# Optimization experiments

Measured on AMD Instinct MI355X. Metric: run time of the kernel, lower is better.

The kernel has to match this reference:

```python
import jax, jax.numpy as jnp
import numpy as np

EPS = 1e-5

def conv1d_same(x, w, b):
    # x: [B,C,T], w: [O,I,K], b: [O]
    y = jax.lax.conv_general_dilated(x, w, window_strides=(1,), padding='SAME',
                                     dimension_numbers=('NCH', 'OIH', 'NCH'))
    return y + b[None, :, None]

def bn_eval(x, gamma, beta):
    # running_mean=0, running_var=1 (fresh BatchNorm1d in eval mode)
    inv = 1.0 / jnp.sqrt(1.0 + EPS)
    return x * (gamma * inv)[None, :, None] + beta[None, :, None]

def gelu(x):
    return jax.nn.gelu(x, approximate=False)

def conv_block(x, c1w, c1b, c2w, c2b, g1, be1, g2, be2, skw=None, skb=None):
    res = x if skw is None else jnp.einsum('bct,oc->bot', x, skw[:, :, 0]) + skb[None, :, None]
    h = gelu(bn_eval(conv1d_same(x, c1w, c1b), g1, be1))
    h = bn_eval(conv1d_same(h, c2w, c2b), g2, be2)
    return gelu(h + res)

def setup_inputs() -> dict:
    key = jax.random.key(0)
    ks = jax.random.split(key, 32)
    B, C, T = 1024, 271, 281
    H, H2, E, NCLS, NSUBJ = 128, 256, 16, 1854, 4
    g = lambda i, shape, s=0.02: jax.random.normal(ks[i], shape, dtype=jnp.float32) * s
    inp = {}
    inp['X'] = jax.random.normal(ks[0], (B, C, T), dtype=jnp.float32)
    inp['subject_idxs'] = jax.random.randint(ks[1], (B,), 0, NSUBJ, dtype=jnp.int32)
    inp['attention'] = jax.random.normal(ks[2], (C, C), dtype=jnp.float32)
    inp['sa_w'] = g(3, (H, C), 0.05)
    inp['sa_b'] = jnp.zeros((H,), jnp.float32)
    inp['subj_w'] = g(4, (NSUBJ, H, H), 0.05)
    inp['subj_b'] = jnp.zeros((NSUBJ, H), jnp.float32)
    # block1: 128->128 (identity skip)
    inp['b1_c1w'] = g(5, (H, H, 3)); inp['b1_c1b'] = jnp.zeros((H,), jnp.float32)
    inp['b1_c2w'] = g(6, (H, H, 3)); inp['b1_c2b'] = jnp.zeros((H,), jnp.float32)
    inp['b1_g1'] = jnp.ones((H,), jnp.float32); inp['b1_be1'] = jnp.zeros((H,), jnp.float32)
    inp['b1_g2'] = jnp.ones((H,), jnp.float32); inp['b1_be2'] = jnp.zeros((H,), jnp.float32)
    # block2: 128->256 (1x1 conv skip)
    inp['b2_c1w'] = g(7, (H2, H, 3)); inp['b2_c1b'] = jnp.zeros((H2,), jnp.float32)
    inp['b2_c2w'] = g(8, (H2, H2, 3)); inp['b2_c2b'] = jnp.zeros((H2,), jnp.float32)
    inp['b2_g1'] = jnp.ones((H2,), jnp.float32); inp['b2_be1'] = jnp.zeros((H2,), jnp.float32)
    inp['b2_g2'] = jnp.ones((H2,), jnp.float32); inp['b2_be2'] = jnp.zeros((H2,), jnp.float32)
    inp['b2_skw'] = g(9, (H2, H, 1)); inp['b2_skb'] = jnp.zeros((H2,), jnp.float32)
    # block3: 256->256 (identity skip)
    inp['b3_c1w'] = g(10, (H2, H2, 3)); inp['b3_c1b'] = jnp.zeros((H2,), jnp.float32)
    inp['b3_c2w'] = g(11, (H2, H2, 3)); inp['b3_c2b'] = jnp.zeros((H2,), jnp.float32)
    inp['b3_g1'] = jnp.ones((H2,), jnp.float32); inp['b3_be1'] = jnp.zeros((H2,), jnp.float32)
    inp['b3_g2'] = jnp.ones((H2,), jnp.float32); inp['b3_be2'] = jnp.zeros((H2,), jnp.float32)
    # subject embedding + head
    inp['emb'] = g(12, (NSUBJ, E), 1.0)
    inp['head_w1'] = g(13, (H, H2 + E), 0.05); inp['head_b1'] = jnp.zeros((H,), jnp.float32)
    inp['head_w2'] = g(14, (NCLS, H), 0.05); inp['head_b2'] = jnp.zeros((NCLS,), jnp.float32)
    return inp

def reference(X, subject_idxs, attention, sa_w, sa_b, subj_w, subj_b,
              b1_c1w, b1_c1b, b1_c2w, b1_c2b, b1_g1, b1_be1, b1_g2, b1_be2,
              b2_c1w, b2_c1b, b2_c2w, b2_c2b, b2_g1, b2_be1, b2_g2, b2_be2, b2_skw, b2_skb,
              b3_c1w, b3_c1b, b3_c2w, b3_c2b, b3_g1, b3_be1, b3_g2, b3_be2,
              emb, head_w1, head_b1, head_w2, head_b2):
    # SpatialAttention
    attn = jax.nn.softmax(attention, axis=1)            # [C,C]
    x = jnp.einsum('bct,ic->bit', X, attn)              # [B,C,T]
    x = jnp.einsum('bit,oi->bot', x, sa_w) + sa_b[None, :, None]  # [B,H,T]
    # Per-subject 1x1 conv: batched gather of weights instead of python loop
    Ws = subj_w[subject_idxs]                           # [B,H,H]
    bs = subj_b[subject_idxs]                           # [B,H]
    x = jnp.einsum('bct,boc->bot', x, Ws) + bs[:, :, None]
    # ConvBlock stack
    x = conv_block(x, b1_c1w, b1_c1b, b1_c2w, b1_c2b, b1_g1, b1_be1, b1_g2, b1_be2)
    x = conv_block(x, b2_c1w, b2_c1b, b2_c2w, b2_c2b, b2_g1, b2_be1, b2_g2, b2_be2, b2_skw, b2_skb)
    x = conv_block(x, b3_c1w, b3_c1b, b3_c2w, b3_c2b, b3_g1, b3_be1, b3_g2, b3_be2)
    # Head: global avg pool over time, concat subject embedding, MLP
    x = jnp.mean(x, axis=2)                             # [B,2H]
    x = jnp.concatenate([x, emb[subject_idxs]], axis=1) # [B,2H+E]
    h = jax.nn.relu(x @ head_w1.T + head_b1)
    return h @ head_w2.T + head_b2                      # [B,num_classes]
```

## Files before the change

kernel.cpp:

```cpp
#include <hip/hip_runtime.h>
#include <hip/hip_bf16.h>
#include <math.h>

constexpr int Bz = 1024;
constexpr int C0 = 271;
constexpr int CP0 = 288;
constexpr int Tt = 281;
constexpr int TR = 292;
constexpr int H1 = 128;
constexpr int H2 = 256;
constexpr int NCLS = 1854;
constexpr int ED = 16;
constexpr float BN_INV = 0.9999950000374996f;

typedef __attribute__((ext_vector_type(8))) short s16x8;
typedef __attribute__((ext_vector_type(16))) float f32x16;

__device__ __forceinline__ float gelu_f(float v) {
    return 0.5f * v * (1.0f + erff(v * 0.7071067811865475f));
}
__device__ __forceinline__ float bf2f(short s) {
    return __builtin_bit_cast(float, ((unsigned int)(unsigned short)s) << 16);
}
__device__ __forceinline__ short f2bf(float f) {
    return __builtin_bit_cast(short, __float2bfloat16(f));
}

typedef unsigned int u32;
typedef const __attribute__((address_space(1))) u32 gu32;
typedef __attribute__((address_space(3))) u32 lu32;

__device__ __forceinline__ void gl16(const void* g, void* l) {
    __builtin_amdgcn_global_load_lds((gu32*)(uintptr_t)g, (lu32*)(uintptr_t)l, 16, 0, 0);
}
template<int N> __device__ __forceinline__ void waitv() {
    asm volatile("s_waitcnt vmcnt(%0)" :: "i"(N) : "memory");
}
__device__ __forceinline__ void hard_barrier() {
    __builtin_amdgcn_sched_barrier(0);
    __builtin_amdgcn_s_barrier();
    __builtin_amdgcn_sched_barrier(0);
}


__global__ void zrows_k(short* base, int C) {
    const int b = blockIdx.x;
    const int n = 11 * (C / 8);
    for (int i = threadIdx.x; i < n; i += 256) {
        int ri = i / (C / 8), c8 = i - ri * (C / 8);
        int row = (ri == 0) ? 0 : 281 + ri;
        *(int4*)(base + ((size_t)b * TR + row) * C + c8 * 8) = make_int4(0, 0, 0, 0);
    }
}

__global__ void softmax_rows_k(const float* __restrict__ a, float* __restrict__ o, int n) {
    __shared__ float red[256];
    const int row = blockIdx.x, tid = threadIdx.x;
    const float* r = a + (size_t)row * n;
    float m = -1e30f;
    for (int i = tid; i < n; i += 256) m = fmaxf(m, r[i]);
    red[tid] = m; __syncthreads();
    for (int s = 128; s > 0; s >>= 1) { if (tid < s) red[tid] = fmaxf(red[tid], red[tid + s]); __syncthreads(); }
    m = red[0]; __syncthreads();
    float acc = 0.f;
    for (int i = tid; i < n; i += 256) acc += expf(r[i] - m);
    red[tid] = acc; __syncthreads();
    for (int s = 128; s > 0; s >>= 1) { if (tid < s) red[tid] += red[tid + s]; __syncthreads(); }
    const float inv = 1.0f / red[0];
    for (int i = tid; i < n; i += 256) o[(size_t)row * n + i] = expf(r[i] - m) * inv;
}

__global__ void gemm_M_k(const float* __restrict__ sa_w, const float* __restrict__ attnS,
                         float* __restrict__ M) {
    int idx = blockIdx.x * 256 + threadIdx.x;
    if (idx >= H1 * C0) return;
    int o = idx / C0, c = idx - o * C0;
    float s = 0.f;
    for (int i = 0; i < C0; ++i) s = fmaf(sa_w[(size_t)o * C0 + i], attnS[(size_t)i * C0 + c], s);
    M[idx] = s;
}

__global__ void wfrag_k(const float* __restrict__ w, short* __restrict__ out,
                        int CIN, int O, int K, int NC) {
    int idx = blockIdx.x * 256 + threadIdx.x;
    int OB32 = O / 32;
    int total = NC * K * OB32 * 2 * 512;
    if (idx >= total) return;
    int j = idx & 7, lane = (idx >> 3) & 63, kk = (idx >> 9) & 1, r = idx >> 10;
    int ob = r % OB32, r2 = r / OB32;
    int k = r2 % K, cc = r2 / K;
    int o = ob * 32 + (lane & 31);
    int c = cc * 32 + kk * 16 + (lane >> 5) * 8 + j;
    float v = (c < CIN) ? w[((size_t)o * CIN + c) * K + k] : 0.f;
    out[idx] = f2bf(v);
}

__global__ void msubA_k(const float* __restrict__ subj_w, const float* __restrict__ M,
                        short* __restrict__ out) {
    int idx = blockIdx.x * 256 + threadIdx.x;
    const int per_s = 9 * 1 * 4 * 2 * 512;
    if (idx >= 4 * per_s) return;
    int s = idx / per_s, rem = idx % per_s;
    int j = rem & 7, lane = (rem >> 3) & 63, kk = (rem >> 9) & 1, r = rem >> 10;
    int ob = r % 4, cc = r / 4;
    int o = ob * 32 + (lane & 31);
    int c = cc * 32 + kk * 16 + (lane >> 5) * 8 + j;
    float a = 0.f;
    if (c < C0) {
        const float* wr = subj_w + ((size_t)s * 128 + o) * 128;
        for (int h = 0; h < 128; ++h) a = fmaf(wr[h], M[(size_t)h * C0 + c], a);
    }
    out[idx] = f2bf(a);
}

__global__ void biasS_k(const float* __restrict__ subj_w, const float* __restrict__ sa_b,
                        const float* __restrict__ subj_b, float* __restrict__ biasS) {
    int idx = blockIdx.x * 256 + threadIdx.x;
    if (idx >= 4 * H1) return;
    int s = idx >> 7, o = idx & 127;
    const float* wr = subj_w + ((size_t)s * H1 + o) * H1;
    float a = subj_b[idx];
    for (int h = 0; h < H1; ++h) a = fmaf(wr[h], sa_b[h], a);
    biasS[idx] = a;
}

__global__ void xpose_k(const float* __restrict__ X, short* __restrict__ xT) {
    __shared__ float tile[32][33];
    int b = blockIdx.z;
    int t0 = blockIdx.x * 32, c0 = blockIdx.y * 32;
    int tx = threadIdx.x, ty = threadIdx.y;
    #pragma unroll
    for (int i = 0; i < 4; ++i) {
        int c = c0 + ty + i * 8, t = t0 + tx;
        float v = 0.f;
        if (c < C0 && t < Tt) v = X[((size_t)b * C0 + c) * Tt + t];
        tile[ty + i * 8][tx] = v;
    }
    __syncthreads();
    #pragma unroll
    for (int i = 0; i < 4; ++i) {
        int t = t0 + ty + i * 8, c = c0 + tx;
        if (t < Tt) xT[((size_t)b * TR + t + 1) * CP0 + c] = f2bf(tile[tx][ty + i * 8]);
    }
}


template<int NCCp, int ROWUp, int NW, int NCH>
__device__ __forceinline__ void conv_stage(
    const short* slabg, int XC, int cubase, char* lds, int wv, int lane)
{
    constexpr int ROWB = ROWUp * 16;
    for (int i = wv; i < NCH; i += NW) {
        int pos = i * 1024 + lane * 16;
        int rl = pos / ROWB;
        int up = (pos - rl * ROWB) >> 4;
        if (rl > 291) rl = 291;
        int ul = up ^ (rl & 7);
        int srcu = (ul < NCCp * 4) ? ul : 0;
        gl16(slabg + (size_t)rl * XC + (cubase + srcu) * 8, lds + i * 1024);
    }
}

template<int K, int CCB, int NPH, int ROWU, int OB32>
__device__ __forceinline__ void conv_phases(
    f32x16 (&acc)[2][3], const short* __restrict__ wb, const char* Xb,
    int tg, int lane, int l31, int hi, int wvo)
{
    constexpr int ROWB = ROWU * 16;
    constexpr int ROFF = 1 - (K - 1) / 2;
    s16x8 ab[2][4];
    #pragma unroll
    for (int i = 0; i < 4; ++i) {
        int ci = ((CCB * K + 0) * OB32 + wvo * 2 + (i >> 1)) * 2 + (i & 1);
        ab[0][i] = *(const s16x8*)(wb + (size_t)ci * 512 + lane * 8);
    }
    #pragma unroll
    for (int p = 0; p < NPH; ++p) {
        const int k  = p % K;
        const int cl = p / K;
        if (p + 1 < NPH) {
            const int cn = CCB + (p + 1) / K, kn = (p + 1) % K;
            #pragma unroll
            for (int i = 0; i < 4; ++i) {
                int ci = ((cn * K + kn) * OB32 + wvo * 2 + (i >> 1)) * 2 + (i & 1);
                ab[(p + 1) & 1][i] = *(const s16x8*)(wb + (size_t)ci * 512 + lane * 8);
            }
        }
        s16x8 bf[2][3];
        #pragma unroll
        for (int kk = 0; kk < 2; ++kk)
            #pragma unroll
            for (int ts = 0; ts < 3; ++ts) {
                int rl = tg + ts * 32 + l31 + k + ROFF;
                bf[kk][ts] = *(const s16x8*)(Xb + (size_t)rl * ROWB +
                               (((cl * 4 + kk * 2 + hi) ^ (rl & 7)) << 4));
            }
        hard_barrier();
        __builtin_amdgcn_s_setprio(1);
        #pragma unroll
        for (int ts = 0; ts < 3; ++ts)
            #pragma unroll
            for (int kk = 0; kk < 2; ++kk) {
                acc[0][ts] = __builtin_amdgcn_mfma_f32_32x32x16_bf16(ab[p & 1][kk],     bf[kk][ts], acc[0][ts], 0, 0, 0);
                acc[1][ts] = __builtin_amdgcn_mfma_f32_32x32x16_bf16(ab[p & 1][2 + kk], bf[kk][ts], acc[1][ts], 0, 0, 0);
            }
        __builtin_amdgcn_s_setprio(0);
        hard_barrier();
    }
}

template<int K, int NCC_A, int ROWU_A, int NCC_B, int ROWU_B,
         int O_BLK, int NOW, int NB, bool GELU, bool HASRES, bool POOL>
__global__ __launch_bounds__(NOW * NB * 192)
void convPH(const short* __restrict__ xin, int XC,
            const short* __restrict__ wfrag,
            const float* __restrict__ bias,
            const float* __restrict__ gamma, const float* __restrict__ beta,
            const short* __restrict__ res, short* __restrict__ outp,
            float* __restrict__ pooled,
            const int* __restrict__ sidx, int wsub, int bsub)
{
    constexpr int NW    = NOW * NB * 3;
    constexpr int NT    = NW * 64;
    constexpr int OB32  = O_BLK / 32;
    constexpr int SLABB = ((292 * ROWU_A * 16) + 1023) & ~1023;
    constexpr int NCH_A = SLABB / 1024;
    constexpr int NCH_B = (292 * ROWU_B * 16 + 1023) / 1024;
    constexpr int O2    = O_BLK * 2;

    __shared__ __align__(16) char smem[NB * SLABB];

    const int b0   = blockIdx.x * NB;
    const int tid  = threadIdx.x;
    const int lane = tid & 63, wv = tid >> 6;
    const int l31  = lane & 31, hi = lane >> 5;
    const int bqw  = wv / (NOW * 3);
    const int w2   = wv % (NOW * 3);
    const int wvt  = w2 / NOW;
    const int wvo  = w2 % NOW;
    const int tg   = wvt * 96;

    int subj = sidx ? sidx[b0] : 0;
    const short* wb = wfrag + (size_t)subj * wsub;
    const float* bb = bias + (size_t)subj * bsub;

    f32x16 acc[2][3];
    #pragma unroll
    for (int i = 0; i < 2; ++i)
        #pragma unroll
        for (int j = 0; j < 3; ++j)
            #pragma unroll
            for (int e = 0; e < 16; ++e) acc[i][j][e] = 0.f;

    #pragma unroll
    for (int b = 0; b < NB; ++b)
        conv_stage<NCC_A, ROWU_A, NW, NCH_A>(
            xin + (size_t)(b0 + b) * TR * XC, XC, 0, smem + b * SLABB, wv, lane);
    waitv<0>();
    hard_barrier();

    const char* Xb = smem + bqw * SLABB;
    conv_phases<K, 0, NCC_A * K, ROWU_A, OB32>(acc, wb, Xb, tg, lane, l31, hi, wvo);

    if constexpr (NCC_B > 0) {
        #pragma unroll
        for (int b = 0; b < NB; ++b)
            conv_stage<NCC_B, ROWU_B, NW, NCH_B>(
                xin + (size_t)(b0 + b) * TR * XC, XC, NCC_A * 4, smem + b * SLABB, wv, lane);
        waitv<0>();
        hard_barrier();
        conv_phases<K, NCC_A, NCC_B * K, ROWU_B, OB32>(acc, wb, Xb, tg, lane, l31, hi, wvo);
    }

    constexpr int RCH = O_BLK / 8;
    float ps[8];
    if constexpr (POOL) {
        #pragma unroll
        for (int j = 0; j < 8; ++j) ps[j] = 0.f;
    }
    for (int g = 0; g < 3; ++g) {
        __syncthreads();
        if (wvt == g) {
            #pragma unroll
            for (int os = 0; os < 2; ++os) {
                #pragma unroll
                for (int rq = 0; rq < 4; ++rq) {
                    #pragma unroll
                    for (int rp = 0; rp < 2; ++rp) {
                        const int oc = wvo * 64 + os * 32 + 8 * rq + rp * 2 + 4 * hi;
                        const float bv0 = bb[oc], bv1 = bb[oc + 1];
                        const float g0 = gamma ? gamma[oc] * BN_INV : 1.f;
                        const float g1 = gamma ? gamma[oc + 1] * BN_INV : 1.f;
                        const float e0 = beta ? beta[oc] : 0.f;
                        const float e1 = beta ? beta[oc + 1] : 0.f;
                        const int r0 = rq * 4 + rp * 2;
                        #pragma unroll
                        for (int ts = 0; ts < 3; ++ts) {
                            float v0 = (acc[os][ts][r0] + bv0) * g0 + e0;
                            float v1 = (acc[os][ts][r0 + 1] + bv1) * g1 + e1;
                            int tl = ts * 32 + l31;
                            int byte = (bqw * 96 + tl) * O2 + ((oc * 2) ^ ((tl & 15) << 4));
                            __hip_bfloat162 pk;
                            pk.x = __float2bfloat16(v0);
                            pk.y = __float2bfloat16(v1);
                            *(__hip_bfloat162*)(smem + byte) = pk;
                        }
                    }
                }
            }
        }
        __syncthreads();
        for (int qq = tid; qq < NB * 96 * RCH; qq += NT) {
            int bql = qq / (96 * RCH), rem = qq - bql * (96 * RCH);
            int r = rem / RCH, cp = rem - r * RCH;
            int t = g * 96 + r;
            if (t >= Tt) continue;
            s16x8 hv = *(const s16x8*)(smem + (bql * 96 + r) * O2 + ((cp * 16) ^ ((r & 15) << 4)));
            size_t orow = ((size_t)(b0 + bql) * TR + t + 1) * O_BLK + cp * 8;
            s16x8 rv;
            if (HASRES) rv = *(const s16x8*)(res + orow);
            if constexpr (POOL) {
                #pragma unroll
                for (int j = 0; j < 8; ++j) {
                    float v = bf2f(hv[j]);
                    if (HASRES) v += bf2f(rv[j]);
                    if (GELU) v = gelu_f(v);
                    ps[j] += v;
                }
            } else {
                s16x8 ov;
                #pragma unroll
                for (int j = 0; j < 8; ++j) {
                    float v = bf2f(hv[j]);
                    if (HASRES) v += bf2f(rv[j]);
                    if (GELU) v = gelu_f(v);
                    ov[j] = f2bf(v);
                }
                *(s16x8*)(outp + orow) = ov;
            }
        }
    }

    if constexpr (POOL) {
        constexpr int NRED = NT / RCH;
        float* part = (float*)(smem + 96 * (size_t)O2);
        __syncthreads();
        #pragma unroll
        for (int j = 0; j < 8; ++j) part[tid * 8 + j] = ps[j];
        __syncthreads();
        if (tid < O_BLK) {
            int cp = tid >> 3, j = tid & 7;
            float s = 0.f;
            for (int r = 0; r < NRED; ++r) s += part[(cp + RCH * r) * 8 + j];
            pooled[(size_t)b0 * H2 + tid] = s * (1.0f / 281.0f);
        }
    }
}


__global__ void head1_k(const float* __restrict__ pooled, const float* __restrict__ emb,
                        const int* __restrict__ sidx, const float* __restrict__ w1,
                        const float* __restrict__ b1, float* __restrict__ hout) {
    int idx = blockIdx.x * 256 + threadIdx.x;
    if (idx >= Bz * H1) return;
    int b = idx >> 7, j = idx & 127;
    const float* wr = w1 + (size_t)j * (H2 + ED);
    const float* pr = pooled + (size_t)b * H2;
    float a = b1[j];
    for (int i = 0; i < H2; ++i) a = fmaf(pr[i], wr[i], a);
    const float* er = emb + (size_t)sidx[b] * ED;
    #pragma unroll
    for (int e = 0; e < ED; ++e) a = fmaf(er[e], wr[H2 + e], a);
    hout[idx] = fmaxf(a, 0.f);
}

__global__ __launch_bounds__(256)
void head2_k(const float* __restrict__ h, const float* __restrict__ w2,
             const float* __restrict__ b2, float* __restrict__ out) {
    const int n0 = blockIdx.x * 64;
    const int b0 = blockIdx.y * 16;
    __shared__ float hs[16][128];
    __shared__ float w2s[64][129];
    const int tid = threadIdx.x;
    for (int idx = tid; idx < 16 * 128; idx += 256) {
        int bl = idx >> 7, j = idx & 127;
        hs[bl][j] = h[(size_t)(b0 + bl) * H1 + j];
    }
    for (int idx = tid; idx < 64 * 128; idx += 256) {
        int nl = idx >> 7, j = idx & 127;
        int n = n0 + nl;
        w2s[nl][j] = (n < NCLS) ? w2[(size_t)n * H1 + j] : 0.f;
    }
    __syncthreads();
    const int nl = tid & 63, bg = tid >> 6;
    float acc[4] = {0.f, 0.f, 0.f, 0.f};
    for (int j = 0; j < 128; ++j) {
        const float wv = w2s[nl][j];
        #pragma unroll
        for (int bb = 0; bb < 4; ++bb) acc[bb] = fmaf(wv, hs[bg * 4 + bb][j], acc[bb]);
    }
    const int n = n0 + nl;
    if (n < NCLS) {
        const float bv = b2[n];
        #pragma unroll
        for (int bb = 0; bb < 4; ++bb)
            out[(size_t)(b0 + bg * 4 + bb) * NCLS + n] = acc[bb] + bv;
    }
}


extern "C" void kernel_launch(void* const* d_in, const int* in_sizes, int n_in,
                              void* d_out, int out_size, void* d_ws, size_t ws_size,
                              hipStream_t stream) {
    const float* X      = (const float*)d_in[0];
    const int*   sidx   = (const int*)  d_in[1];
    const float* attn   = (const float*)d_in[2];
    const float* sa_w   = (const float*)d_in[3];
    const float* sa_b   = (const float*)d_in[4];
    const float* subj_w = (const float*)d_in[5];
    const float* subj_b = (const float*)d_in[6];
    const float* b1c1w = (const float*)d_in[7];  const float* b1c1b = (const float*)d_in[8];
    const float* b1c2w = (const float*)d_in[9];  const float* b1c2b = (const float*)d_in[10];
    const float* b1g1  = (const float*)d_in[11]; const float* b1be1 = (const float*)d_in[12];
    const float* b1g2  = (const float*)d_in[13]; const float* b1be2 = (const float*)d_in[14];
    const float* b2c1w = (const float*)d_in[15]; const float* b2c1b = (const float*)d_in[16];
    const float* b2c2w = (const float*)d_in[17]; const float* b2c2b = (const float*)d_in[18];
    const float* b2g1  = (const float*)d_in[19]; const float* b2be1 = (const float*)d_in[20];
    const float* b2g2  = (const float*)d_in[21]; const float* b2be2 = (const float*)d_in[22];
    const float* b2skw = (const float*)d_in[23]; const float* b2skb = (const float*)d_in[24];
    const float* b3c1w = (const float*)d_in[25]; const float* b3c1b = (const float*)d_in[26];
    const float* b3c2w = (const float*)d_in[27]; const float* b3c2b = (const float*)d_in[28];
    const float* b3g1  = (const float*)d_in[29]; const float* b3be1 = (const float*)d_in[30];
    const float* b3g2  = (const float*)d_in[31]; const float* b3be2 = (const float*)d_in[32];
    const float* emb   = (const float*)d_in[33];
    const float* hw1   = (const float*)d_in[34]; const float* hb1 = (const float*)d_in[35];
    const float* hw2   = (const float*)d_in[36]; const float* hb2 = (const float*)d_in[37];
    float* out = (float*)d_out;
    (void)in_sizes; (void)n_in; (void)out_size; (void)ws_size;

    char* wsp = (char*)d_ws;
    size_t off = 0;
    auto allocF = [&](size_t n) {
        float* p = (float*)(wsp + off);
        off += ((n * sizeof(float)) + 255) & ~(size_t)255;
        return p;
    };
    auto allocS = [&](size_t n) {
        short* p = (short*)(wsp + off);
        off += ((n * sizeof(short)) + 255) & ~(size_t)255;
        return p;
    };
    float* attnS   = allocF((size_t)C0 * C0);
    float* Mmat    = allocF((size_t)H1 * C0);
    float* biasS   = allocF((size_t)4 * H1);
    float* pooled  = allocF((size_t)Bz * H2);
    float* hbuf    = allocF((size_t)Bz * H1);
    short* wStageA = allocS((size_t)4 * 9 * 4 * 2 * 512);
    short* wp_b1c1 = allocS((size_t)4 * 3 * 4 * 2 * 512);
    short* wp_b1c2 = allocS((size_t)4 * 3 * 4 * 2 * 512);
    short* wp_skip = allocS((size_t)4 * 1 * 8 * 2 * 512);
    short* wp_b2c1 = allocS((size_t)4 * 3 * 8 * 2 * 512);
    short* wp_b2c2 = allocS((size_t)8 * 3 * 8 * 2 * 512);
    short* wp_b3c1 = allocS((size_t)8 * 3 * 8 * 2 * 512);
    short* wp_b3c2 = allocS((size_t)8 * 3 * 8 * 2 * 512);
    short* xT   = allocS((size_t)Bz * TR * CP0 + 64);
    short* bufP = allocS((size_t)Bz * TR * H1);
    short* bufQ = allocS((size_t)Bz * TR * H1);
    short* bufR = allocS((size_t)Bz * TR * H2);
    short* bufS = allocS((size_t)Bz * TR * H2);

    zrows_k<<<Bz, 256, 0, stream>>>(xT, CP0);
    zrows_k<<<Bz, 256, 0, stream>>>(bufP, H1);
    zrows_k<<<Bz, 256, 0, stream>>>(bufQ, H1);
    zrows_k<<<Bz, 256, 0, stream>>>(bufR, H2);
    zrows_k<<<Bz, 256, 0, stream>>>(bufS, H2);

    softmax_rows_k<<<C0, 256, 0, stream>>>(attn, attnS, C0);
    gemm_M_k<<<(H1 * C0 + 255) / 256, 256, 0, stream>>>(sa_w, attnS, Mmat);
    msubA_k<<<(4 * 36864 + 255) / 256, 256, 0, stream>>>(subj_w, Mmat, wStageA);
    biasS_k<<<2, 256, 0, stream>>>(subj_w, sa_b, subj_b, biasS);
    wfrag_k<<<(4*3*4*2*512 + 255) / 256, 256, 0, stream>>>(b1c1w, wp_b1c1, 128, 128, 3, 4);
    wfrag_k<<<(4*3*4*2*512 + 255) / 256, 256, 0, stream>>>(b1c2w, wp_b1c2, 128, 128, 3, 4);
    wfrag_k<<<(4*1*8*2*512 + 255) / 256, 256, 0, stream>>>(b2skw, wp_skip, 128, 256, 1, 4);
    wfrag_k<<<(4*3*8*2*512 + 255) / 256, 256, 0, stream>>>(b2c1w, wp_b2c1, 128, 256, 3, 4);
    wfrag_k<<<(8*3*8*2*512 + 255) / 256, 256, 0, stream>>>(b2c2w, wp_b2c2, 256, 256, 3, 8);
    wfrag_k<<<(8*3*8*2*512 + 255) / 256, 256, 0, stream>>>(b3c1w, wp_b3c1, 256, 256, 3, 8);
    wfrag_k<<<(8*3*8*2*512 + 255) / 256, 256, 0, stream>>>(b3c2w, wp_b3c2, 256, 256, 3, 8);
    xpose_k<<<dim3(9, 9, Bz), dim3(32, 8), 0, stream>>>(X, xT);

    convPH<1, 5, 24, 4, 16, 128, 2, 1, false, false, false><<<Bz, 384, 0, stream>>>(
        xT, CP0, wStageA, biasS, nullptr, nullptr, nullptr, bufP, nullptr, sidx, 36864, 128);
    convPH<3, 4, 16, 0, 0, 128, 2, 2, true, false, false><<<Bz / 2, 768, 0, stream>>>(
        bufP, H1, wp_b1c1, b1c1b, b1g1, b1be1, nullptr, bufQ, nullptr, nullptr, 0, 0);
    convPH<3, 4, 16, 0, 0, 128, 2, 2, true, true, false><<<Bz / 2, 768, 0, stream>>>(
        bufQ, H1, wp_b1c2, b1c2b, b1g2, b1be2, bufP, bufP, nullptr, nullptr, 0, 0);
    convPH<1, 4, 16, 0, 0, 256, 4, 1, false, false, false><<<Bz, 768, 0, stream>>>(
        bufP, H1, wp_skip, b2skb, nullptr, nullptr, nullptr, bufS, nullptr, nullptr, 0, 0);
    convPH<3, 4, 16, 0, 0, 256, 4, 1, true, false, false><<<Bz, 768, 0, stream>>>(
        bufP, H1, wp_b2c1, b2c1b, b2g1, b2be1, nullptr, bufR, nullptr, nullptr, 0, 0);
    convPH<3, 8, 32, 0, 0, 256, 4, 1, true, true, false><<<Bz, 768, 0, stream>>>(
        bufR, H2, wp_b2c2, b2c2b, b2g2, b2be2, bufS, bufS, nullptr, nullptr, 0, 0);
    convPH<3, 8, 32, 0, 0, 256, 4, 1, true, false, false><<<Bz, 768, 0, stream>>>(
        bufS, H2, wp_b3c1, b3c1b, b3g1, b3be1, nullptr, bufR, nullptr, nullptr, 0, 0);
    convPH<3, 8, 32, 0, 0, 256, 4, 1, true, true, true><<<Bz, 768, 0, stream>>>(
        bufR, H2, wp_b3c2, b3c2b, b3g2, b3be2, bufS, nullptr, pooled, nullptr, 0, 0);

    head1_k<<<(Bz * H1 + 255) / 256, 256, 0, stream>>>(pooled, emb, sidx, hw1, hb1, hbuf);
    head2_k<<<dim3((NCLS + 63) / 64, Bz / 16), 256, 0, stream>>>(hbuf, hw2, hb2, out);
}
```

Before: 1.367 ms.

## Restructure conv kernels into sliced LDS staging with split-wait overlap and 512-thread blocks

```diff
diff --git a/kernel.cpp b/kernel.cpp
--- a/kernel.cpp
+++ b/kernel.cpp
@@ -98,7 +98,7 @@
 __global__ void msubA_k(const float* __restrict__ subj_w, const float* __restrict__ M,
                         short* __restrict__ out) {
     int idx = blockIdx.x * 256 + threadIdx.x;
-    const int per_s = 9 * 1 * 4 * 2 * 512;
+    const int per_s = 10 * 1 * 4 * 2 * 512;
     if (idx >= 4 * per_s) return;
     int s = idx / per_s, rem = idx % per_s;
     int j = rem & 7, lane = (rem >> 3) & 63, kk = (rem >> 9) & 1, r = rem >> 10;
@@ -145,178 +145,165 @@
 }
 
 
-template<int NCCp, int ROWUp, int NW, int NCH>
-__device__ __forceinline__ void conv_stage(
-    const short* slabg, int XC, int cubase, char* lds, int wv, int lane)
+constexpr int SLICEB = 38912;
+
+template<int K, int CCB, int NCCP, int SOFF, int OB32, int NTS>
+__device__ __forceinline__ void dw_compute(
+    f32x16 (&acc)[NTS], const short* __restrict__ wb, const char* Xb,
+    int TS0, int lane, int l31, int hi, int wvo)
 {
-    constexpr int ROWB = ROWUp * 16;
-    for (int i = wv; i < NCH; i += NW) {
-        int pos = i * 1024 + lane * 16;
-        int rl = pos / ROWB;
-        int up = (pos - rl * ROWB) >> 4;
-        if (rl > 291) rl = 291;
-        int ul = up ^ (rl & 7);
-        int srcu = (ul < NCCp * 4) ? ul : 0;
-        gl16(slabg + (size_t)rl * XC + (cubase + srcu) * 8, lds + i * 1024);
-    }
-}
-
-template<int K, int CCB, int NPH, int ROWU, int OB32>
-__device__ __forceinline__ void conv_phases(
-    f32x16 (&acc)[2][3], const short* __restrict__ wb, const char* Xb,
-    int tg, int lane, int l31, int hi, int wvo)
-{
-    constexpr int ROWB = ROWU * 16;
     constexpr int ROFF = 1 - (K - 1) / 2;
-    s16x8 ab[2][4];
     #pragma unroll
-    for (int i = 0; i < 4; ++i) {
-        int ci = ((CCB * K + 0) * OB32 + wvo * 2 + (i >> 1)) * 2 + (i & 1);
-        ab[0][i] = *(const s16x8*)(wb + (size_t)ci * 512 + lane * 8);
-    }
-    #pragma unroll
-    for (int p = 0; p < NPH; ++p) {
-        const int k  = p % K;
-        const int cl = p / K;
-        if (p + 1 < NPH) {
-            const int cn = CCB + (p + 1) / K, kn = (p + 1) % K;
+    for (int c = 0; c < NCCP; ++c) {
+        const int cc = CCB + c;
+        s16x8 a[K][2];
+        #pragma unroll
+        for (int k = 0; k < K; ++k)
             #pragma unroll
-            for (int i = 0; i < 4; ++i) {
-                int ci = ((cn * K + kn) * OB32 + wvo * 2 + (i >> 1)) * 2 + (i & 1);
-                ab[(p + 1) & 1][i] = *(const s16x8*)(wb + (size_t)ci * 512 + lane * 8);
-            }
-        }
-        s16x8 bf[2][3];
-        #pragma unroll
-        for (int kk = 0; kk < 2; ++kk)
+            for (int kk = 0; kk < 2; ++kk)
+                a[k][kk] = *(const s16x8*)(wb +
+                    (size_t)(((cc * K + k) * OB32 + wvo) * 2 + kk) * 512 + lane * 8);
+        __builtin_amdgcn_s_setprio(1);
+        #pragma unroll
+        for (int k = 0; k < K; ++k)
             #pragma unroll
-            for (int ts = 0; ts < 3; ++ts) {
-                int rl = tg + ts * 32 + l31 + k + ROFF;
-                bf[kk][ts] = *(const s16x8*)(Xb + (size_t)rl * ROWB +
-                               (((cl * 4 + kk * 2 + hi) ^ (rl & 7)) << 4));
-            }
-        hard_barrier();
-        __builtin_amdgcn_s_setprio(1);
-        #pragma unroll
-        for (int ts = 0; ts < 3; ++ts)
-            #pragma unroll
-            for (int kk = 0; kk < 2; ++kk) {
-                acc[0][ts] = __builtin_amdgcn_mfma_f32_32x32x16_bf16(ab[p & 1][kk],     bf[kk][ts], acc[0][ts], 0, 0, 0);
-                acc[1][ts] = __builtin_amdgcn_mfma_f32_32x32x16_bf16(ab[p & 1][2 + kk], bf[kk][ts], acc[1][ts], 0, 0, 0);
-            }
+            for (int kk = 0; kk < 2; ++kk)
+                #pragma unroll
+                for (int t = 0; t < NTS; ++t) {
+                    int ts = TS0 + t;
+                    if (ts < 9) {
+                        int rl = ts * 32 + l31 + k + ROFF;
+                        s16x8 bv = *(const s16x8*)(Xb + ((cc >> 1) - SOFF) * SLICEB +
+                            rl * 128 + ((((cc & 1) * 4 + kk * 2 + hi) ^ (rl & 7)) << 4));
+                        acc[t] = __builtin_amdgcn_mfma_f32_32x32x16_bf16(a[k][kk], bv, acc[t], 0, 0, 0);
+                    }
+                }
         __builtin_amdgcn_s_setprio(0);
-        hard_barrier();
-    }
-}
-
-template<int K, int NCC_A, int ROWU_A, int NCC_B, int ROWU_B,
-         int O_BLK, int NOW, int NB, bool GELU, bool HASRES, bool POOL>
-__global__ __launch_bounds__(NOW * NB * 192)
-void convPH(const short* __restrict__ xin, int XC,
-            const short* __restrict__ wfrag,
+    }
+}
+
+template<int K, int NCC, int O_BLK, int NB, int NTH, int PH1,
+         bool GELU, bool HASRES, bool POOL>
+__global__ __launch_bounds__(512, 2)
+void convDW(const short* __restrict__ xin, int XC,
+            const short* __restrict__ wf,
             const float* __restrict__ bias,
             const float* __restrict__ gamma, const float* __restrict__ beta,
             const short* __restrict__ res, short* __restrict__ outp,
             float* __restrict__ pooled,
             const int* __restrict__ sidx, int wsub, int bsub)
 {
-    constexpr int NW    = NOW * NB * 3;
-    constexpr int NT    = NW * 64;
-    constexpr int OB32  = O_BLK / 32;
-    constexpr int SLABB = ((292 * ROWU_A * 16) + 1023) & ~1023;
-    constexpr int NCH_A = SLABB / 1024;
-    constexpr int NCH_B = (292 * ROWU_B * 16 + 1023) / 1024;
-    constexpr int O2    = O_BLK * 2;
+    constexpr int NOS  = O_BLK / 32;
+    constexpr int NSL1 = PH1 / 2;
+    constexpr int NSL2 = (NCC - PH1) / 2;
+    constexpr int SLABB = NSL1 * SLICEB;
+    constexpr int NTS  = (NTH == 2) ? 5 : 9;
+    constexpr int O2   = O_BLK * 2;
+    constexpr int RCH  = O_BLK / 8;
+    constexpr int SECTS = (SLABB / (32 * O2)) < 9 ? (SLABB / (32 * O2)) : 9;
+    constexpr int NSEC  = (9 + SECTS - 1) / SECTS;
+    constexpr int NW1   = (NB * (NSL1 - 1) * 38) / 8;
 
     __shared__ __align__(16) char smem[NB * SLABB];
 
     const int b0   = blockIdx.x * NB;
     const int tid  = threadIdx.x;
-    const int lane = tid & 63, wv = tid >> 6;
+    const int lane = tid & 63, w = tid >> 6;
     const int l31  = lane & 31, hi = lane >> 5;
-    const int bqw  = wv / (NOW * 3);
-    const int w2   = wv % (NOW * 3);
-    const int wvt  = w2 / NOW;
-    const int wvo  = w2 % NOW;
-    const int tg   = wvt * 96;
+    const int bq   = w / (NTH * NOS);
+    const int r1   = w % (NTH * NOS);
+    const int th   = r1 / NOS;
+    const int wvo  = r1 % NOS;
+    const int TS0  = (NTH == 2) ? th * 5 : 0;
 
     int subj = sidx ? sidx[b0] : 0;
-    const short* wb = wfrag + (size_t)subj * wsub;
+    const short* wb = wf + (size_t)subj * wsub;
     const float* bb = bias + (size_t)subj * bsub;
 
-    f32x16 acc[2][3];
+    f32x16 acc[NTS];
     #pragma unroll
-    for (int i = 0; i < 2; ++i)
-        #pragma unroll
-        for (int j = 0; j < 3; ++j)
-            #pragma unroll
-            for (int e = 0; e < 16; ++e) acc[i][j][e] = 0.f;
-
-    #pragma unroll
-    for (int b = 0; b < NB; ++b)
-        conv_stage<NCC_A, ROWU_A, NW, NCH_A>(
-            xin + (size_t)(b0 + b) * TR * XC, XC, 0, smem + b * SLABB, wv, lane);
-    waitv<0>();
-    hard_barrier();
-
-    const char* Xb = smem + bqw * SLABB;
-    conv_phases<K, 0, NCC_A * K, ROWU_A, OB32>(acc, wb, Xb, tg, lane, l31, hi, wvo);
-
-    if constexpr (NCC_B > 0) {
-        #pragma unroll
-        for (int b = 0; b < NB; ++b)
-            conv_stage<NCC_B, ROWU_B, NW, NCH_B>(
-                xin + (size_t)(b0 + b) * TR * XC, XC, NCC_A * 4, smem + b * SLABB, wv, lane);
-        waitv<0>();
+    for (int i = 0; i < NTS; ++i)
+        #pragma unroll
+        for (int e = 0; e < 16; ++e) acc[i][e] = 0.f;
+
+    auto stage = [&](int gu0, int nsl) {
+        const int total = NB * nsl * 38;
+        for (int i = w; i < total; i += 8) {
+            int sb = i / (nsl * 38);
+            int j  = i % (nsl * 38);
+            int s  = j / 38, jj = j - s * 38;
+            int pos = jj * 1024 + lane * 16;
+            int r  = pos >> 7;
+            int up = (pos >> 4) & 7;
+            int us = up ^ (r & 7);
+            int rr = r > 291 ? 291 : r;
+            gl16(xin + ((size_t)(b0 + sb) * TR + rr) * XC + (gu0 + s * 8 + us) * 8,
+                 smem + (size_t)sb * SLABB + s * SLICEB + jj * 1024);
+        }
+    };
+
+    const char* Xb = smem + (size_t)bq * SLABB;
+
+    stage(0, NSL1);
+    waitv<NW1>(); hard_barrier();
+    dw_compute<K, 0, 2, 0, NOS, NTS>(acc, wb, Xb, TS0, lane, l31, hi, wvo);
+    waitv<0>(); hard_barrier();
+    dw_compute<K, 2, PH1 - 2, 0, NOS, NTS>(acc, wb, Xb, TS0, lane, l31, hi, wvo);
+
+    if constexpr (PH1 < NCC) {
         hard_barrier();
-        conv_phases<K, NCC_A, NCC_B * K, ROWU_B, OB32>(acc, wb, Xb, tg, lane, l31, hi, wvo);
-    }
-
-    constexpr int RCH = O_BLK / 8;
+        stage(PH1 * 4, NSL2);
+        waitv<0>(); hard_barrier();
+        dw_compute<K, PH1, NCC - PH1, PH1 / 2, NOS, NTS>(acc, wb, Xb, TS0, lane, l31, hi, wvo);
+    }
+
     float ps[8];
     if constexpr (POOL) {
         #pragma unroll
         for (int j = 0; j < 8; ++j) ps[j] = 0.f;
     }
-    for (int g = 0; g < 3; ++g) {
-        __syncthreads();
-        if (wvt == g) {
-            #pragma unroll
-            for (int os = 0; os < 2; ++os) {
+
+    for (int g = 0; g < NSEC; ++g) {
+        hard_barrier();
+        #pragma unroll
+        for (int t = 0; t < NTS; ++t) {
+            int ts = TS0 + t;
+            if (ts < 9 && ts >= g * SECTS && ts < (g + 1) * SECTS) {
                 #pragma unroll
-                for (int rq = 0; rq < 4; ++rq) {
+                for (int rq = 0; rq < 4; ++rq)
                     #pragma unroll
                     for (int rp = 0; rp < 2; ++rp) {
-                        const int oc = wvo * 64 + os * 32 + 8 * rq + rp * 2 + 4 * hi;
+                        const int oc = wvo * 32 + 8 * rq + rp * 2 + 4 * hi;
                         const float bv0 = bb[oc], bv1 = bb[oc + 1];
                         const float g0 = gamma ? gamma[oc] * BN_INV : 1.f;
                         const float g1 = gamma ? gamma[oc + 1] * BN_INV : 1.f;
                         const float e0 = beta ? beta[oc] : 0.f;
                         const float e1 = beta ? beta[oc + 1] : 0.f;
                         const int r0 = rq * 4 + rp * 2;
-                        #pragma unroll
-                        for (int ts = 0; ts < 3; ++ts) {
-                            float v0 = (acc[os][ts][r0] + bv0) * g0 + e0;
-                            float v1 = (acc[os][ts][r0 + 1] + bv1) * g1 + e1;
-                            int tl = ts * 32 + l31;
-                            int byte = (bqw * 96 + tl) * O2 + ((oc * 2) ^ ((tl & 15) << 4));
-                            __hip_bfloat162 pk;
-                            pk.x = __float2bfloat16(v0);
-                            pk.y = __float2bfloat16(v1);
-                            *(__hip_bfloat162*)(smem + byte) = pk;
-                        }
+                        float v0 = (acc[t][r0] + bv0) * g0 + e0;
+                        float v1 = (acc[t][r0 + 1] + bv1) * g1 + e1;
+                        int tl = ts * 32 + l31;
+                        int rowsec = tl - g * SECTS * 32;
+                        int byte = bq * SLABB + rowsec * O2 + ((oc * 2) ^ ((tl & 15) << 4));
+                        __hip_bfloat162 pk;
+                        pk.x = __float2bfloat16(v0);
+                        pk.y = __float2bfloat16(v1);
+                        *(__hip_bfloat162*)(smem + byte) = pk;
                     }
-                }
             }
         }
-        __syncthreads();
-        for (int qq = tid; qq < NB * 96 * RCH; qq += NT) {
-            int bql = qq / (96 * RCH), rem = qq - bql * (96 * RCH);
-            int r = rem / RCH, cp = rem - r * RCH;
-            int t = g * 96 + r;
-            if (t >= Tt) continue;
-            s16x8 hv = *(const s16x8*)(smem + (bql * 96 + r) * O2 + ((cp * 16) ^ ((r & 15) << 4)));
-            size_t orow = ((size_t)(b0 + bql) * TR + t + 1) * O_BLK + cp * 8;
+        hard_barrier();
+        const int tsend = (g + 1) * SECTS < 9 ? (g + 1) * SECTS : 9;
+        const int secrows = (tsend - g * SECTS) * 32;
+        for (int q = tid; q < NB * secrows * RCH; q += 512) {
+            int sb = q / (secrows * RCH);
+            int rem = q - sb * (secrows * RCH);
+            int rr = rem / RCH, cp = rem - rr * RCH;
+            int tt = g * SECTS * 32 + rr;
+            if (tt >= Tt) continue;
+            s16x8 hv = *(const s16x8*)(smem + (size_t)sb * SLABB + rr * O2 +
+                                       ((cp * 16) ^ ((rr & 15) << 4)));
+            size_t orow = ((size_t)(b0 + sb) * TR + tt + 1) * O_BLK + cp * 8;
             s16x8 rv;
             if (HASRES) rv = *(const s16x8*)(res + orow);
             if constexpr (POOL) {
@@ -342,12 +329,12 @@
     }
 
     if constexpr (POOL) {
-        constexpr int NRED = NT / RCH;
-        float* part = (float*)(smem + 96 * (size_t)O2);
-        __syncthreads();
+        constexpr int NRED = 512 / RCH;
+        float* part = (float*)smem;
+        hard_barrier();
         #pragma unroll
         for (int j = 0; j < 8; ++j) part[tid * 8 + j] = ps[j];
-        __syncthreads();
+        hard_barrier();
         if (tid < O_BLK) {
             int cp = tid >> 3, j = tid & 7;
             float s = 0.f;
@@ -455,7 +442,7 @@
     float* biasS   = allocF((size_t)4 * H1);
     float* pooled  = allocF((size_t)Bz * H2);
     float* hbuf    = allocF((size_t)Bz * H1);
-    short* wStageA = allocS((size_t)4 * 9 * 4 * 2 * 512);
+    short* wStageA = allocS((size_t)4 * 10 * 4 * 2 * 512);
     short* wp_b1c1 = allocS((size_t)4 * 3 * 4 * 2 * 512);
     short* wp_b1c2 = allocS((size_t)4 * 3 * 4 * 2 * 512);
     short* wp_skip = allocS((size_t)4 * 1 * 8 * 2 * 512);
@@ -477,7 +464,7 @@
 
     softmax_rows_k<<<C0, 256, 0, stream>>>(attn, attnS, C0);
     gemm_M_k<<<(H1 * C0 + 255) / 256, 256, 0, stream>>>(sa_w, attnS, Mmat);
-    msubA_k<<<(4 * 36864 + 255) / 256, 256, 0, stream>>>(subj_w, Mmat, wStageA);
+    msubA_k<<<(4 * 40960 + 255) / 256, 256, 0, stream>>>(subj_w, Mmat, wStageA);
     biasS_k<<<2, 256, 0, stream>>>(subj_w, sa_b, subj_b, biasS);
     wfrag_k<<<(4*3*4*2*512 + 255) / 256, 256, 0, stream>>>(b1c1w, wp_b1c1, 128, 128, 3, 4);
     wfrag_k<<<(4*3*4*2*512 + 255) / 256, 256, 0, stream>>>(b1c2w, wp_b1c2, 128, 128, 3, 4);
@@ -488,21 +475,21 @@
     wfrag_k<<<(8*3*8*2*512 + 255) / 256, 256, 0, stream>>>(b3c2w, wp_b3c2, 256, 256, 3, 8);
     xpose_k<<<dim3(9, 9, Bz), dim3(32, 8), 0, stream>>>(X, xT);
 
-    convPH<1, 5, 24, 4, 16, 128, 2, 1, false, false, false><<<Bz, 384, 0, stream>>>(
-        xT, CP0, wStageA, biasS, nullptr, nullptr, nullptr, bufP, nullptr, sidx, 36864, 128);
-    convPH<3, 4, 16, 0, 0, 128, 2, 2, true, false, false><<<Bz / 2, 768, 0, stream>>>(
+    convDW<1, 10, 128, 1, 2, 6, false, false, false><<<Bz, 512, 0, stream>>>(
+        xT, CP0, wStageA, biasS, nullptr, nullptr, nullptr, bufP, nullptr, sidx, 40960, 128);
+    convDW<3, 4, 128, 2, 1, 4, true, false, false><<<Bz / 2, 512, 0, stream>>>(
         bufP, H1, wp_b1c1, b1c1b, b1g1, b1be1, nullptr, bufQ, nullptr, nullptr, 0, 0);
-    convPH<3, 4, 16, 0, 0, 128, 2, 2, true, true, false><<<Bz / 2, 768, 0, stream>>>(
+    convDW<3, 4, 128, 2, 1, 4, true, true, false><<<Bz / 2, 512, 0, stream>>>(
         bufQ, H1, wp_b1c2, b1c2b, b1g2, b1be2, bufP, bufP, nullptr, nullptr, 0, 0);
-    convPH<1, 4, 16, 0, 0, 256, 4, 1, false, false, false><<<Bz, 768, 0, stream>>>(
+    convDW<1, 4, 256, 1, 1, 4, false, false, false><<<Bz, 512, 0, stream>>>(
         bufP, H1, wp_skip, b2skb, nullptr, nullptr, nullptr, bufS, nullptr, nullptr, 0, 0);
-    convPH<3, 4, 16, 0, 0, 256, 4, 1, true, false, false><<<Bz, 768, 0, stream>>>(
+    convDW<3, 4, 256, 1, 1, 4, true, false, false><<<Bz, 512, 0, stream>>>(
         bufP, H1, wp_b2c1, b2c1b, b2g1, b2be1, nullptr, bufR, nullptr, nullptr, 0, 0);
-    convPH<3, 8, 32, 0, 0, 256, 4, 1, true, true, false><<<Bz, 768, 0, stream>>>(
+    convDW<3, 8, 256, 1, 1, 8, true, true, false><<<Bz, 512, 0, stream>>>(
         bufR, H2, wp_b2c2, b2c2b, b2g2, b2be2, bufS, bufS, nullptr, nullptr, 0, 0);
-    convPH<3, 8, 32, 0, 0, 256, 4, 1, true, false, false><<<Bz, 768, 0, stream>>>(
+    convDW<3, 8, 256, 1, 1, 8, true, false, false><<<Bz, 512, 0, stream>>>(
         bufS, H2, wp_b3c1, b3c1b, b3g1, b3be1, nullptr, bufR, nullptr, nullptr, 0, 0);
-    convPH<3, 8, 32, 0, 0, 256, 4, 1, true, true, true><<<Bz, 768, 0, stream>>>(
+    convDW<3, 8, 256, 1, 1, 8, true, true, true><<<Bz, 512, 0, stream>>>(
         bufR, H2, wp_b3c2, b3c2b, b3g2, b3be2, bufS, nullptr, pooled, nullptr, 0, 0);
 
     head1_k<<<(Bz * H1 + 255) / 256, 256, 0, stream>>>(pooled, emb, sidx, hw1, hb1, hbuf);
```

Result: slower. 1.443 ms (+5.6%).
